# Performance work log

Hardware: AMD Instinct MI355X
Metric: run time of the kernel (lower is better)

Reference implementation:

```python
import jax, jax.numpy as jnp
import numpy as np


def _linear_init(key, fan_in, fan_out):
    bound = 1.0 / np.sqrt(fan_in)
    k1, k2 = jax.random.split(key)
    w = jax.random.uniform(k1, (fan_in, fan_out), jnp.float32, -bound, bound)
    b = jax.random.uniform(k2, (fan_out,), jnp.float32, -bound, bound)
    return w, b


def setup_inputs() -> dict:
    key = jax.random.key(0)
    ks = jax.random.split(key, 8)
    B, T, K, F, H, D = 4, 64, 50, 6, 128, 256
    states = jax.random.normal(ks[0], (B, T, K, F), jnp.float32)
    masks = (jax.random.uniform(ks[1], (B, T, K)) < 0.9).astype(jnp.float32)
    w_a, b_a = _linear_init(ks[2], F, H)              # agent_encoder
    w_r1, b_r1 = _linear_init(ks[3], 2 * H + 3, H)    # relation_encoder layer 1
    w_r2, b_r2 = _linear_init(ks[4], H, H)            # relation_encoder layer 2
    w_g, b_g = _linear_init(ks[5], 2 * H, H)          # graph_aggregation
    w_f1, b_f1 = _linear_init(ks[6], H, D)            # final_encoder layer 1
    w_f2, b_f2 = _linear_init(ks[7], D, D)            # final_encoder layer 2
    return dict(states=states, masks=masks, w_a=w_a, b_a=b_a,
                w_r1=w_r1, b_r1=b_r1, w_r2=w_r2, b_r2=b_r2,
                w_g=w_g, b_g=b_g, w_f1=w_f1, b_f1=b_f1, w_f2=w_f2, b_f2=b_f2)


def _safe_norm(r):
    # sqrt(sum r^2) with well-defined gradient at 0 (torch.norm convention)
    sq = jnp.sum(r * r, axis=-1, keepdims=True)
    return jnp.where(sq == 0, 0.0, jnp.sqrt(jnp.where(sq == 0, 1.0, sq)))


def reference(states, masks, w_a, b_a, w_r1, b_r1, w_r2, b_r2,
              w_g, b_g, w_f1, b_f1, w_f2, b_f2):
    B, T, K, F = states.shape
    H = w_a.shape[1]
    s = states.reshape(B * T, K, F)            # [N,K,F]
    m = masks.reshape(B * T, K)                # [N,K]
    agent_feat = jax.nn.relu(s @ w_a + b_a)    # [N,K,H] (dropout = identity, eval)
    pos = s[..., :2]
    vel = s[..., 2:4]
    # rel[n,i,j] = quantity_j - quantity_i
    rel_pos = pos[:, None, :, :] - pos[:, :, None, :]   # [N,K,K,2]
    rel_vel = vel[:, None, :, :] - vel[:, :, None, :]
    dist = _safe_norm(rel_pos)                          # [N,K,K,1]
    rx, ry = rel_pos[..., 0:1], rel_pos[..., 1:2]
    safe_x = jnp.where((rx == 0) & (ry == 0), 1.0, rx)  # atan2(0,1)=atan2(0,0)=0
    angle = jnp.arctan2(ry, safe_x)
    speed_diff = _safe_norm(rel_vel)
    geo = jnp.concatenate([dist, angle, speed_diff], axis=-1)  # [N,K,K,3]
    # Split the first relation linear instead of materializing the
    # [N,K,K,2H+3] concat: cat([f_i, f_j, geo]) @ w_r1 == f@w_i + f@w_j + geo@w_geo
    x_i = agent_feat @ w_r1[:H]            # [N,K,H]
    x_j = agent_feat @ w_r1[H:2 * H]       # [N,K,H]
    g = geo @ w_r1[2 * H:] + b_r1          # [N,K,K,H]
    h = jax.nn.relu(x_i[:, :, None, :] + x_j[:, None, :, :] + g)
    rel_feat = h @ w_r2 + b_r2             # [N,K,K,H]
    mask_pairs = m[:, :, None] * m[:, None, :]          # [N,i,j]
    rel_feat = rel_feat * mask_pairs[..., None]
    denom = jnp.maximum(mask_pairs.sum(axis=2, keepdims=True), 1.0)  # [N,K,1]
    agg = rel_feat.sum(axis=2) / denom                  # [N,K,H]
    combined = jax.nn.relu(agent_feat @ w_g[:H] + agg @ w_g[H:] + b_g)  # [N,K,H]
    me = m[..., None]
    pooled = (combined * me).sum(axis=1) / jnp.maximum(me.sum(axis=1), 1.0)  # [N,H]
    latent = jax.nn.relu(pooled @ w_f1 + b_f1) @ w_f2 + b_f2                 # [N,D]
    return latent.reshape(B, T, -1)
```

## Files before the change

kernel.cpp:

```cpp
#include <hip/hip_runtime.h>

#define KA 50
#define KP 52
#define H 128
#define D 256
#define NBLK 256
#define BLOCK 1024
#define NG 8
#define RPT 7
#define STRD 136

#define WS_WI 0
#define WS_WJ 32
#define WS_WR2 64
#define WS_WG 96
#define NFRAG 160

typedef __attribute__((ext_vector_type(8))) short bf16x8;
typedef __attribute__((ext_vector_type(4))) float f32x4;

__device__ __forceinline__ float bf2f(unsigned short u) {
  return __uint_as_float(((unsigned)u) << 16);
}
__device__ __forceinline__ unsigned short f2bf(float f) {
  unsigned u = __float_as_uint(f);
  u = (u + 0x7FFFu + ((u >> 16) & 1u)) >> 16;
  return (unsigned short)u;
}
__device__ __forceinline__ float rlf(float v, int l) {
  return __int_as_float(__builtin_amdgcn_readlane(__float_as_int(v), l));
}

__global__ void pack_weights(const float* __restrict__ w_r1,
                             const float* __restrict__ w_r2,
                             const float* __restrict__ w_g,
                             unsigned short* __restrict__ wp) {
  const int t = blockIdx.x * 256 + threadIdx.x;
  if (t >= NFRAG * 64) return;
  const int f = t >> 6, lane = t & 63;
  const float* W; int rowbase, sf;
  if (f < 64)       { W = w_r1; rowbase = (f < 32) ? 0 : 128; sf = f & 31; }
  else if (f < 96)  { W = w_r2; rowbase = 0; sf = f - 64; }
  else              { W = w_g;  rowbase = 0; sf = f - 96; }
  const int kt = sf >> 3, ctl = sf & 7;
  const int col = ctl * 16 + (lane & 15);
  const int k0  = rowbase + kt * 32 + (lane >> 4) * 8;
  unsigned short v[8];
  #pragma unroll
  for (int j = 0; j < 8; ++j) v[j] = f2bf(W[(k0 + j) * H + col]);
  #pragma unroll
  for (int j = 0; j < 8; ++j) wp[(size_t)t * 8 + j] = v[j];
}

struct alignas(16) Smem {
  unsigned short af[KP * STRD];
  unsigned short xi[KP * STRD];
  unsigned short xj[KP * H];
  unsigned short hsum[KP * STRD];
  float red[1024];
  float pooled[H];
  float latent1[D];
  float s[KA][6];
  float m[64];
  float cnta[KP];
  float invden[KP];
  float cnt;
};

__global__ void __launch_bounds__(BLOCK) rpe_kernel(
    const float* __restrict__ states, const float* __restrict__ masks,
    const float* __restrict__ w_a,  const float* __restrict__ b_a,
    const float* __restrict__ w_r1, const float* __restrict__ b_r1,
    const float* __restrict__ b_r2,
    const float* __restrict__ b_g,
    const float* __restrict__ w_f1, const float* __restrict__ b_f1,
    const float* __restrict__ w_f2, const float* __restrict__ b_f2,
    const unsigned short* __restrict__ wp,
    float* __restrict__ out) {
  __shared__ Smem sh;
  const int n = blockIdx.x;
  const int tid = threadIdx.x;
  const int c = tid & (H - 1);
  const int bg = tid >> 7;
  const int wid = tid >> 6, lane = tid & 63;
  const int ct = wid & 7;
  const int rtb = (wid >> 3) * 2;
  const int fr = lane & 15;
  const int fkg = lane >> 4;

  {
    if (tid < KA * 6) ((float*)sh.s)[tid] = states[(size_t)n * (KA * 6) + tid];
    if (tid < 64) sh.m[tid] = (tid < KA) ? masks[(size_t)n * KA + tid] : 0.f;
    if (tid < 2 * H) {
      const int r5 = KA + (tid >> 7), cc = tid & (H - 1);
      sh.af[r5 * STRD + cc] = 0;
      sh.hsum[r5 * STRD + cc] = 0;
    }
  }
  __syncthreads();
  if (tid == 0) {
    float cs = 0.f;
    for (int b = 0; b < KA; ++b) cs += sh.m[b];
    sh.cnt = cs;
  }
  {
    const float bac = b_a[c];
    const float w0 = w_a[0*H+c], w1 = w_a[1*H+c], w2 = w_a[2*H+c];
    const float w3 = w_a[3*H+c], w4 = w_a[4*H+c], w5 = w_a[5*H+c];
    #pragma unroll
    for (int r = 0; r < RPT; ++r) {
      const int a = bg + NG * r;
      if (a < KA) {
        const float* srow = sh.s[a];
        float v = fmaf(srow[0], w0, fmaf(srow[1], w1, fmaf(srow[2], w2,
                  fmaf(srow[3], w3, fmaf(srow[4], w4, fmaf(srow[5], w5, bac))))));
        sh.af[a * STRD + c] = f2bf(fmaxf(v, 0.f));
      }
    }
  }
  __syncthreads();
  if (tid < KP) {
    const float ca = (tid < KA) ? sh.m[tid] * sh.cnt : 0.f;
    sh.cnta[tid] = ca;
    sh.invden[tid] = 1.0f / fmaxf(ca, 1.0f);
  }

  {
    f32x4 ci0 = {0,0,0,0}, ci1 = {0,0,0,0}, cj0 = {0,0,0,0}, cj1 = {0,0,0,0};
    #pragma unroll
    for (int kt = 0; kt < 4; ++kt) {
      const bf16x8 Bi = *(const bf16x8*)&wp[(size_t)((WS_WI + kt*8 + ct) * 64 + lane) * 8];
      const bf16x8 Bj = *(const bf16x8*)&wp[(size_t)((WS_WJ + kt*8 + ct) * 64 + lane) * 8];
      const bf16x8 A0 = *(const bf16x8*)&sh.af[(rtb*16 + fr) * STRD + kt*32 + fkg*8];
      const bf16x8 A1 = *(const bf16x8*)&sh.af[((rtb+1)*16 + fr) * STRD + kt*32 + fkg*8];
      ci0 = __builtin_amdgcn_mfma_f32_16x16x32_bf16(A0, Bi, ci0, 0, 0, 0);
      ci1 = __builtin_amdgcn_mfma_f32_16x16x32_bf16(A1, Bi, ci1, 0, 0, 0);
      cj0 = __builtin_amdgcn_mfma_f32_16x16x32_bf16(A0, Bj, cj0, 0, 0, 0);
      cj1 = __builtin_amdgcn_mfma_f32_16x16x32_bf16(A1, Bj, cj1, 0, 0, 0);
    }
    const int col = ct * 16 + fr;
    #pragma unroll
    for (int rt2 = 0; rt2 < 2; ++rt2) {
      const f32x4 vi = rt2 ? ci1 : ci0;
      const f32x4 vj = rt2 ? cj1 : cj0;
      #pragma unroll
      for (int g = 0; g < 4; ++g) {
        const int r = (rtb + rt2) * 16 + fkg * 4 + g;
        if (r < KP) {
          sh.xi[r * STRD + col] = f2bf(vi[g]);
          sh.xj[r * H + col]    = f2bf(vj[g]);
        }
      }
    }
  }
  __syncthreads();

  {
    const int c0 = 2 * lane;
    const float wgd0  = w_r1[256*H + c0], wgd1  = w_r1[256*H + c0+1];
    const float wgan0 = w_r1[257*H + c0], wgan1 = w_r1[257*H + c0+1];
    const float wgs0  = w_r1[258*H + c0], wgs1  = w_r1[258*H + c0+1];
    const float br10  = b_r1[c0],         br11  = b_r1[c0+1];
    const int bl = (lane < KA) ? lane : (KA - 1);
    const float pbx = sh.s[bl][0], pby = sh.s[bl][1];
    const float pvx = sh.s[bl][2], pvy = sh.s[bl][3];
    const float mb  = sh.m[lane];

    float dG[3], aG[3], sG[3], b0v[3], b1v[3], h0v[3], h1v[3];
    #pragma unroll
    for (int r = 0; r < 3; ++r) {
      const int ar = wid + 16 * r;
      const float rx  = pbx - sh.s[ar][0], ry  = pby - sh.s[ar][1];
      const float dvx = pvx - sh.s[ar][2], dvy = pvy - sh.s[ar][3];
      dG[r] = sqrtf(fmaf(rx, rx, ry * ry));
      const float sx = (rx == 0.f && ry == 0.f) ? 1.f : rx;
      aG[r] = atan2f(ry, sx);
      sG[r] = sqrtf(fmaf(dvx, dvx, dvy * dvy));
      const unsigned xip = *(const unsigned*)&sh.xi[ar * STRD + c0];
      b0v[r] = bf2f((unsigned short)xip) + br10;
      b1v[r] = bf2f((unsigned short)(xip >> 16)) + br11;
      h0v[r] = 0.f; h1v[r] = 0.f;
    }
    #pragma unroll 10
    for (int b = 0; b < KA; ++b) {
      const unsigned xjp = *(const unsigned*)&sh.xj[b * H + c0];
      const float xj0 = __uint_as_float(xjp << 16);
      const float xj1 = __uint_as_float(xjp & 0xFFFF0000u);
      const float mm = rlf(mb, b);
      #pragma unroll
      for (int r = 0; r < 3; ++r) {
        const float dd = rlf(dG[r], b), aa = rlf(aG[r], b), ss = rlf(sG[r], b);
        float t0 = fmaf(dd, wgd0, b0v[r]); t0 = fmaf(aa, wgan0, t0);
        t0 = fmaf(ss, wgs0, t0);  t0 += xj0;
        float t1 = fmaf(dd, wgd1, b1v[r]); t1 = fmaf(aa, wgan1, t1);
        t1 = fmaf(ss, wgs1, t1);  t1 += xj1;
        h0v[r] = fmaf(mm, fmaxf(t0, 0.f), h0v[r]);
        h1v[r] = fmaf(mm, fmaxf(t1, 0.f), h1v[r]);
      }
    }
    #pragma unroll
    for (int r = 0; r < 3; ++r) {
      const int ar = wid + 16 * r;
      const float ma = sh.m[ar];
      const float g0 = h0v[r] * ma, g1 = h1v[r] * ma;
      *(unsigned*)&sh.hsum[ar * STRD + c0] =
          (unsigned)f2bf(g0) | ((unsigned)f2bf(g1) << 16);
    }
    if (wid < 2) {
      const int ar = 48 + wid;
      const float rx  = pbx - sh.s[ar][0], ry  = pby - sh.s[ar][1];
      const float dvx = pvx - sh.s[ar][2], dvy = pvy - sh.s[ar][3];
      const float dGt = sqrtf(fmaf(rx, rx, ry * ry));
      const float sx  = (rx == 0.f && ry == 0.f) ? 1.f : rx;
      const float aGt = atan2f(ry, sx);
      const float sGt = sqrtf(fmaf(dvx, dvx, dvy * dvy));
      const unsigned xip = *(const unsigned*)&sh.xi[ar * STRD + c0];
      const float b0t = bf2f((unsigned short)xip) + br10;
      const float b1t = bf2f((unsigned short)(xip >> 16)) + br11;
      float h0 = 0.f, h1 = 0.f;
      #pragma unroll 10
      for (int b = 0; b < KA; ++b) {
        const unsigned xjp = *(const unsigned*)&sh.xj[b * H + c0];
        const float xj0 = __uint_as_float(xjp << 16);
        const float xj1 = __uint_as_float(xjp & 0xFFFF0000u);
        const float mm = rlf(mb, b);
        const float dd = rlf(dGt, b), aa = rlf(aGt, b), ss = rlf(sGt, b);
        float t0 = fmaf(dd, wgd0, b0t); t0 = fmaf(aa, wgan0, t0);
        t0 = fmaf(ss, wgs0, t0);  t0 += xj0;
        float t1 = fmaf(dd, wgd1, b1t); t1 = fmaf(aa, wgan1, t1);
        t1 = fmaf(ss, wgs1, t1);  t1 += xj1;
        h0 = fmaf(mm, fmaxf(t0, 0.f), h0);
        h1 = fmaf(mm, fmaxf(t1, 0.f), h1);
      }
      const float ma = sh.m[ar];
      const float g0 = h0 * ma, g1 = h1 * ma;
      *(unsigned*)&sh.hsum[ar * STRD + c0] =
          (unsigned)f2bf(g0) | ((unsigned)f2bf(g1) << 16);
    }
  }
  __syncthreads();

  {
    f32x4 a0 = {0,0,0,0}, a1 = {0,0,0,0};
    #pragma unroll
    for (int kt = 0; kt < 4; ++kt) {
      const bf16x8 B = *(const bf16x8*)&wp[(size_t)((WS_WR2 + kt*8 + ct) * 64 + lane) * 8];
      const bf16x8 A0 = *(const bf16x8*)&sh.hsum[(rtb*16 + fr) * STRD + kt*32 + fkg*8];
      const bf16x8 A1 = *(const bf16x8*)&sh.hsum[((rtb+1)*16 + fr) * STRD + kt*32 + fkg*8];
      a0 = __builtin_amdgcn_mfma_f32_16x16x32_bf16(A0, B, a0, 0, 0, 0);
      a1 = __builtin_amdgcn_mfma_f32_16x16x32_bf16(A1, B, a1, 0, 0, 0);
    }
    const int col = ct * 16 + fr;
    const float br2c = b_r2[col];
    #pragma unroll
    for (int rt2 = 0; rt2 < 2; ++rt2) {
      const f32x4 v = rt2 ? a1 : a0;
      #pragma unroll
      for (int g = 0; g < 4; ++g) {
        const int r = (rtb + rt2) * 16 + fkg * 4 + g;
        if (r < KP) {
          const float val = fmaf(sh.cnta[r], br2c, v[g]) * sh.invden[r];
          sh.xi[r * STRD + col] = f2bf(val);
        }
      }
    }
  }
  __syncthreads();

  {
    f32x4 a0 = {0,0,0,0}, a1 = {0,0,0,0};
    #pragma unroll
    for (int kt = 0; kt < 4; ++kt) {
      const bf16x8 B = *(const bf16x8*)&wp[(size_t)((WS_WG + kt*8 + ct) * 64 + lane) * 8];
      const bf16x8 A0 = *(const bf16x8*)&sh.af[(rtb*16 + fr) * STRD + kt*32 + fkg*8];
      const bf16x8 A1 = *(const bf16x8*)&sh.af[((rtb+1)*16 + fr) * STRD + kt*32 + fkg*8];
      a0 = __builtin_amdgcn_mfma_f32_16x16x32_bf16(A0, B, a0, 0, 0, 0);
      a1 = __builtin_amdgcn_mfma_f32_16x16x32_bf16(A1, B, a1, 0, 0, 0);
    }
    #pragma unroll
    for (int kt = 0; kt < 4; ++kt) {
      const bf16x8 B = *(const bf16x8*)&wp[(size_t)((WS_WG + (kt+4)*8 + ct) * 64 + lane) * 8];
      const bf16x8 A0 = *(const bf16x8*)&sh.xi[(rtb*16 + fr) * STRD + kt*32 + fkg*8];
      const bf16x8 A1 = *(const bf16x8*)&sh.xi[((rtb+1)*16 + fr) * STRD + kt*32 + fkg*8];
      a0 = __builtin_amdgcn_mfma_f32_16x16x32_bf16(A0, B, a0, 0, 0, 0);
      a1 = __builtin_amdgcn_mfma_f32_16x16x32_bf16(A1, B, a1, 0, 0, 0);
    }
    const int col = ct * 16 + fr;
    const float bgc = b_g[col];
    float pv = 0.f;
    #pragma unroll
    for (int rt2 = 0; rt2 < 2; ++rt2) {
      const f32x4 v = rt2 ? a1 : a0;
      #pragma unroll
      for (int g = 0; g < 4; ++g) {
        const int r = (rtb + rt2) * 16 + fkg * 4 + g;
        if (r < KA) {
          pv = fmaf(sh.m[r], fmaxf(v[g] + bgc, 0.f), pv);
        }
      }
    }
    pv += __shfl_xor(pv, 16);
    pv += __shfl_xor(pv, 32);
    if (lane < 16) sh.red[(wid >> 3) * H + col] = pv;
  }
  __syncthreads();
  if (tid < H) {
    const float invp = 1.0f / fmaxf(sh.cnt, 1.0f);
    sh.pooled[tid] = (sh.red[tid] + sh.red[H + tid]) * invp;
  }
  __syncthreads();

  {
    const int d  = tid & (D - 1);
    const int hh = tid >> 8;
    const float* wf = w_f1 + d;
    float acc = 0.f;
    const int k0 = hh * 32;
    #pragma unroll 8
    for (int k = 0; k < 32; ++k)
      acc = fmaf(sh.pooled[k0 + k], wf[(k0 + k) * D], acc);
    sh.red[hh * D + d] = acc;
  }
  __syncthreads();
  if (tid < D) {
    sh.latent1[tid] = fmaxf(sh.red[tid] + sh.red[D + tid] +
                            sh.red[2*D + tid] + sh.red[3*D + tid] +
                            b_f1[tid], 0.f);
  }
  __syncthreads();

  {
    const int d  = tid & (D - 1);
    const int hh = tid >> 8;
    const float* wf = w_f2 + d;
    float acc = 0.f;
    const int k0 = hh * 64;
    #pragma unroll 8
    for (int k = 0; k < 64; ++k)
      acc = fmaf(sh.latent1[k0 + k], wf[(k0 + k) * D], acc);
    sh.red[hh * D + d] = acc;
  }
  __syncthreads();
  if (tid < D) {
    out[(size_t)n * D + tid] = sh.red[tid] + sh.red[D + tid] +
                               sh.red[2*D + tid] + sh.red[3*D + tid] +
                               b_f2[tid];
  }
}

extern "C" void kernel_launch(void* const* d_in, const int* in_sizes, int n_in,
                              void* d_out, int out_size, void* d_ws, size_t ws_size,
                              hipStream_t stream) {
  const float* states = (const float*)d_in[0];
  const float* masks  = (const float*)d_in[1];
  const float* w_a  = (const float*)d_in[2];
  const float* b_a  = (const float*)d_in[3];
  const float* w_r1 = (const float*)d_in[4];
  const float* b_r1 = (const float*)d_in[5];
  const float* w_r2 = (const float*)d_in[6];
  const float* b_r2 = (const float*)d_in[7];
  const float* w_g  = (const float*)d_in[8];
  const float* b_g  = (const float*)d_in[9];
  const float* w_f1 = (const float*)d_in[10];
  const float* b_f1 = (const float*)d_in[11];
  const float* w_f2 = (const float*)d_in[12];
  const float* b_f2 = (const float*)d_in[13];
  float* out = (float*)d_out;
  unsigned short* wp = (unsigned short*)d_ws;

  hipLaunchKernelGGL(pack_weights, dim3((NFRAG * 64 + 255) / 256), dim3(256), 0, stream,
                     w_r1, w_r2, w_g, wp);
  hipLaunchKernelGGL(rpe_kernel, dim3(NBLK), dim3(BLOCK), 0, stream,
                     states, masks, w_a, b_a, w_r1, b_r1, b_r2,
                     b_g, w_f1, b_f1, w_f2, b_f2, wp, out);
}
```

Measured before the change: 42.47 us.

## Hoist weight loads and geometry math ahead of barriers to overlap latency

Global weight loads (w_a, relation geometry weights, MFMA B fragments, final-encoder weights) are issued earlier, before the barriers that precede their use. Pairwise geometry (distance, atan2, speed) is computed during the agent-encoder phase instead of after the x_i/x_j MFMA phase. The first half of the graph-aggregation MFMA is merged into the w_r2 MFMA loop, and the mask count uses a wave shuffle reduction instead of a serial loop on one thread. The aim is to hide global-memory latency and shorten the serial sync stages, at the cost of many more live registers (96 floats for w_f1/w_f2 plus B fragments) in a 1024-thread block, which risks spills.

```diff
diff --git a/kernel.cpp b/kernel.cpp
--- a/kernel.cpp
+++ b/kernel.cpp
@@ -87,6 +87,16 @@
   const int rtb = (wid >> 3) * 2;
   const int fr = lane & 15;
   const int fkg = lane >> 4;
+  const int col = ct * 16 + fr;
+
+  const float bac = b_a[c];
+  const float wa0 = w_a[0*H+c], wa1 = w_a[1*H+c], wa2 = w_a[2*H+c];
+  const float wa3 = w_a[3*H+c], wa4 = w_a[4*H+c], wa5 = w_a[5*H+c];
+  const int c0 = 2 * lane;
+  const float wgd0  = w_r1[256*H + c0], wgd1  = w_r1[256*H + c0+1];
+  const float wgan0 = w_r1[257*H + c0], wgan1 = w_r1[257*H + c0+1];
+  const float wgs0  = w_r1[258*H + c0], wgs1  = w_r1[258*H + c0+1];
+  const float br10  = b_r1[c0],         br11  = b_r1[c0+1];
 
   {
     if (tid < KA * 6) ((float*)sh.s)[tid] = states[(size_t)n * (KA * 6) + tid];
@@ -98,25 +108,56 @@
     }
   }
   __syncthreads();
-  if (tid == 0) {
-    float cs = 0.f;
-    for (int b = 0; b < KA; ++b) cs += sh.m[b];
-    sh.cnt = cs;
-  }
-  {
-    const float bac = b_a[c];
-    const float w0 = w_a[0*H+c], w1 = w_a[1*H+c], w2 = w_a[2*H+c];
-    const float w3 = w_a[3*H+c], w4 = w_a[4*H+c], w5 = w_a[5*H+c];
+  if (wid == 0) {
+    float v = sh.m[lane];
+    v += __shfl_xor(v, 1);  v += __shfl_xor(v, 2);  v += __shfl_xor(v, 4);
+    v += __shfl_xor(v, 8);  v += __shfl_xor(v, 16); v += __shfl_xor(v, 32);
+    if (lane == 0) sh.cnt = v;
+  }
+
+  const int bl = (lane < KA) ? lane : (KA - 1);
+  const float pbx = sh.s[bl][0], pby = sh.s[bl][1];
+  const float pvx = sh.s[bl][2], pvy = sh.s[bl][3];
+  const float mb  = sh.m[lane];
+  float dG[3], aG[3], sG[3];
+  #pragma unroll
+  for (int r = 0; r < 3; ++r) {
+    const int ar = wid + 16 * r;
+    const float rx  = pbx - sh.s[ar][0], ry  = pby - sh.s[ar][1];
+    const float dvx = pvx - sh.s[ar][2], dvy = pvy - sh.s[ar][3];
+    dG[r] = sqrtf(fmaf(rx, rx, ry * ry));
+    const float sx = (rx == 0.f && ry == 0.f) ? 1.f : rx;
+    aG[r] = atan2f(ry, sx);
+    sG[r] = sqrtf(fmaf(dvx, dvx, dvy * dvy));
+  }
+  float dGt = 0.f, aGt = 0.f, sGt = 0.f;
+  if (wid < 2) {
+    const int ar = 48 + wid;
+    const float rx  = pbx - sh.s[ar][0], ry  = pby - sh.s[ar][1];
+    const float dvx = pvx - sh.s[ar][2], dvy = pvy - sh.s[ar][3];
+    dGt = sqrtf(fmaf(rx, rx, ry * ry));
+    const float sx = (rx == 0.f && ry == 0.f) ? 1.f : rx;
+    aGt = atan2f(ry, sx);
+    sGt = sqrtf(fmaf(dvx, dvx, dvy * dvy));
+  }
+
+  {
     #pragma unroll
     for (int r = 0; r < RPT; ++r) {
       const int a = bg + NG * r;
       if (a < KA) {
         const float* srow = sh.s[a];
-        float v = fmaf(srow[0], w0, fmaf(srow[1], w1, fmaf(srow[2], w2,
-                  fmaf(srow[3], w3, fmaf(srow[4], w4, fmaf(srow[5], w5, bac))))));
+        float v = fmaf(srow[0], wa0, fmaf(srow[1], wa1, fmaf(srow[2], wa2,
+                  fmaf(srow[3], wa3, fmaf(srow[4], wa4, fmaf(srow[5], wa5, bac))))));
         sh.af[a * STRD + c] = f2bf(fmaxf(v, 0.f));
       }
     }
+  }
+  bf16x8 Bi[4], Bj[4];
+  #pragma unroll
+  for (int kt = 0; kt < 4; ++kt) {
+    Bi[kt] = *(const bf16x8*)&wp[(size_t)((WS_WI + kt*8 + ct) * 64 + lane) * 8];
+    Bj[kt] = *(const bf16x8*)&wp[(size_t)((WS_WJ + kt*8 + ct) * 64 + lane) * 8];
   }
   __syncthreads();
   if (tid < KP) {
@@ -129,16 +170,13 @@
     f32x4 ci0 = {0,0,0,0}, ci1 = {0,0,0,0}, cj0 = {0,0,0,0}, cj1 = {0,0,0,0};
     #pragma unroll
     for (int kt = 0; kt < 4; ++kt) {
-      const bf16x8 Bi = *(const bf16x8*)&wp[(size_t)((WS_WI + kt*8 + ct) * 64 + lane) * 8];
-      const bf16x8 Bj = *(const bf16x8*)&wp[(size_t)((WS_WJ + kt*8 + ct) * 64 + lane) * 8];
       const bf16x8 A0 = *(const bf16x8*)&sh.af[(rtb*16 + fr) * STRD + kt*32 + fkg*8];
       const bf16x8 A1 = *(const bf16x8*)&sh.af[((rtb+1)*16 + fr) * STRD + kt*32 + fkg*8];
-      ci0 = __builtin_amdgcn_mfma_f32_16x16x32_bf16(A0, Bi, ci0, 0, 0, 0);
-      ci1 = __builtin_amdgcn_mfma_f32_16x16x32_bf16(A1, Bi, ci1, 0, 0, 0);
-      cj0 = __builtin_amdgcn_mfma_f32_16x16x32_bf16(A0, Bj, cj0, 0, 0, 0);
-      cj1 = __builtin_amdgcn_mfma_f32_16x16x32_bf16(A1, Bj, cj1, 0, 0, 0);
-    }
-    const int col = ct * 16 + fr;
+      ci0 = __builtin_amdgcn_mfma_f32_16x16x32_bf16(A0, Bi[kt], ci0, 0, 0, 0);
+      ci1 = __builtin_amdgcn_mfma_f32_16x16x32_bf16(A1, Bi[kt], ci1, 0, 0, 0);
+      cj0 = __builtin_amdgcn_mfma_f32_16x16x32_bf16(A0, Bj[kt], cj0, 0, 0, 0);
+      cj1 = __builtin_amdgcn_mfma_f32_16x16x32_bf16(A1, Bj[kt], cj1, 0, 0, 0);
+    }
     #pragma unroll
     for (int rt2 = 0; rt2 < 2; ++rt2) {
       const f32x4 vi = rt2 ? ci1 : ci0;
@@ -156,26 +194,10 @@
   __syncthreads();
 
   {
-    const int c0 = 2 * lane;
-    const float wgd0  = w_r1[256*H + c0], wgd1  = w_r1[256*H + c0+1];
-    const float wgan0 = w_r1[257*H + c0], wgan1 = w_r1[257*H + c0+1];
-    const float wgs0  = w_r1[258*H + c0], wgs1  = w_r1[258*H + c0+1];
-    const float br10  = b_r1[c0],         br11  = b_r1[c0+1];
-    const int bl = (lane < KA) ? lane : (KA - 1);
-    const float pbx = sh.s[bl][0], pby = sh.s[bl][1];
-    const float pvx = sh.s[bl][2], pvy = sh.s[bl][3];
-    const float mb  = sh.m[lane];
-
-    float dG[3], aG[3], sG[3], b0v[3], b1v[3], h0v[3], h1v[3];
+    float b0v[3], b1v[3], h0v[3], h1v[3];
     #pragma unroll
     for (int r = 0; r < 3; ++r) {
       const int ar = wid + 16 * r;
-      const float rx  = pbx - sh.s[ar][0], ry  = pby - sh.s[ar][1];
-      const float dvx = pvx - sh.s[ar][2], dvy = pvy - sh.s[ar][3];
-      dG[r] = sqrtf(fmaf(rx, rx, ry * ry));
-      const float sx = (rx == 0.f && ry == 0.f) ? 1.f : rx;
-      aG[r] = atan2f(ry, sx);
-      sG[r] = sqrtf(fmaf(dvx, dvx, dvy * dvy));
       const unsigned xip = *(const unsigned*)&sh.xi[ar * STRD + c0];
       b0v[r] = bf2f((unsigned short)xip) + br10;
       b1v[r] = bf2f((unsigned short)(xip >> 16)) + br11;
@@ -208,12 +230,6 @@
     }
     if (wid < 2) {
       const int ar = 48 + wid;
-      const float rx  = pbx - sh.s[ar][0], ry  = pby - sh.s[ar][1];
-      const float dvx = pvx - sh.s[ar][2], dvy = pvy - sh.s[ar][3];
-      const float dGt = sqrtf(fmaf(rx, rx, ry * ry));
-      const float sx  = (rx == 0.f && ry == 0.f) ? 1.f : rx;
-      const float aGt = atan2f(ry, sx);
-      const float sGt = sqrtf(fmaf(dvx, dvx, dvy * dvy));
       const unsigned xip = *(const unsigned*)&sh.xi[ar * STRD + c0];
       const float b0t = bf2f((unsigned short)xip) + br10;
       const float b1t = bf2f((unsigned short)(xip >> 16)) + br11;
@@ -240,17 +256,22 @@
   }
   __syncthreads();
 
+  f32x4 p0 = {0,0,0,0}, p1 = {0,0,0,0};
   {
     f32x4 a0 = {0,0,0,0}, a1 = {0,0,0,0};
     #pragma unroll
     for (int kt = 0; kt < 4; ++kt) {
-      const bf16x8 B = *(const bf16x8*)&wp[(size_t)((WS_WR2 + kt*8 + ct) * 64 + lane) * 8];
-      const bf16x8 A0 = *(const bf16x8*)&sh.hsum[(rtb*16 + fr) * STRD + kt*32 + fkg*8];
-      const bf16x8 A1 = *(const bf16x8*)&sh.hsum[((rtb+1)*16 + fr) * STRD + kt*32 + fkg*8];
-      a0 = __builtin_amdgcn_mfma_f32_16x16x32_bf16(A0, B, a0, 0, 0, 0);
-      a1 = __builtin_amdgcn_mfma_f32_16x16x32_bf16(A1, B, a1, 0, 0, 0);
-    }
-    const int col = ct * 16 + fr;
+      const bf16x8 B4 = *(const bf16x8*)&wp[(size_t)((WS_WR2 + kt*8 + ct) * 64 + lane) * 8];
+      const bf16x8 A0h = *(const bf16x8*)&sh.hsum[(rtb*16 + fr) * STRD + kt*32 + fkg*8];
+      const bf16x8 A1h = *(const bf16x8*)&sh.hsum[((rtb+1)*16 + fr) * STRD + kt*32 + fkg*8];
+      a0 = __builtin_amdgcn_mfma_f32_16x16x32_bf16(A0h, B4, a0, 0, 0, 0);
+      a1 = __builtin_amdgcn_mfma_f32_16x16x32_bf16(A1h, B4, a1, 0, 0, 0);
+      const bf16x8 B5 = *(const bf16x8*)&wp[(size_t)((WS_WG + kt*8 + ct) * 64 + lane) * 8];
+      const bf16x8 A0a = *(const bf16x8*)&sh.af[(rtb*16 + fr) * STRD + kt*32 + fkg*8];
+      const bf16x8 A1a = *(const bf16x8*)&sh.af[((rtb+1)*16 + fr) * STRD + kt*32 + fkg*8];
+      p0 = __builtin_amdgcn_mfma_f32_16x16x32_bf16(A0a, B5, p0, 0, 0, 0);
+      p1 = __builtin_amdgcn_mfma_f32_16x16x32_bf16(A1a, B5, p1, 0, 0, 0);
+    }
     const float br2c = b_r2[col];
     #pragma unroll
     for (int rt2 = 0; rt2 < 2; ++rt2) {
@@ -268,29 +289,19 @@
   __syncthreads();
 
   {
-    f32x4 a0 = {0,0,0,0}, a1 = {0,0,0,0};
-    #pragma unroll
-    for (int kt = 0; kt < 4; ++kt) {
-      const bf16x8 B = *(const bf16x8*)&wp[(size_t)((WS_WG + kt*8 + ct) * 64 + lane) * 8];
-      const bf16x8 A0 = *(const bf16x8*)&sh.af[(rtb*16 + fr) * STRD + kt*32 + fkg*8];
-      const bf16x8 A1 = *(const bf16x8*)&sh.af[((rtb+1)*16 + fr) * STRD + kt*32 + fkg*8];
-      a0 = __builtin_amdgcn_mfma_f32_16x16x32_bf16(A0, B, a0, 0, 0, 0);
-      a1 = __builtin_amdgcn_mfma_f32_16x16x32_bf16(A1, B, a1, 0, 0, 0);
-    }
     #pragma unroll
     for (int kt = 0; kt < 4; ++kt) {
       const bf16x8 B = *(const bf16x8*)&wp[(size_t)((WS_WG + (kt+4)*8 + ct) * 64 + lane) * 8];
       const bf16x8 A0 = *(const bf16x8*)&sh.xi[(rtb*16 + fr) * STRD + kt*32 + fkg*8];
       const bf16x8 A1 = *(const bf16x8*)&sh.xi[((rtb+1)*16 + fr) * STRD + kt*32 + fkg*8];
-      a0 = __builtin_amdgcn_mfma_f32_16x16x32_bf16(A0, B, a0, 0, 0, 0);
-      a1 = __builtin_amdgcn_mfma_f32_16x16x32_bf16(A1, B, a1, 0, 0, 0);
-    }
-    const int col = ct * 16 + fr;
+      p0 = __builtin_amdgcn_mfma_f32_16x16x32_bf16(A0, B, p0, 0, 0, 0);
+      p1 = __builtin_amdgcn_mfma_f32_16x16x32_bf16(A1, B, p1, 0, 0, 0);
+    }
     const float bgc = b_g[col];
     float pv = 0.f;
     #pragma unroll
     for (int rt2 = 0; rt2 < 2; ++rt2) {
-      const f32x4 v = rt2 ? a1 : a0;
+      const f32x4 v = rt2 ? p1 : p0;
       #pragma unroll
       for (int g = 0; g < 4; ++g) {
         const int r = (rtb + rt2) * 16 + fkg * 4 + g;
@@ -303,6 +314,15 @@
     pv += __shfl_xor(pv, 32);
     if (lane < 16) sh.red[(wid >> 3) * H + col] = pv;
   }
+  const int d67 = tid & (D - 1);
+  const int hh67 = tid >> 8;
+  float wf1r[32];
+  {
+    const float* wf = w_f1 + d67;
+    const int k06 = hh67 * 32;
+    #pragma unroll
+    for (int k = 0; k < 32; ++k) wf1r[k] = wf[(k06 + k) * D];
+  }
   __syncthreads();
   if (tid < H) {
     const float invp = 1.0f / fmaxf(sh.cnt, 1.0f);
@@ -311,15 +331,19 @@
   __syncthreads();
 
   {
-    const int d  = tid & (D - 1);
-    const int hh = tid >> 8;
-    const float* wf = w_f1 + d;
     float acc = 0.f;
-    const int k0 = hh * 32;
-    #pragma unroll 8
+    const int k06 = hh67 * 32;
+    #pragma unroll
     for (int k = 0; k < 32; ++k)
-      acc = fmaf(sh.pooled[k0 + k], wf[(k0 + k) * D], acc);
-    sh.red[hh * D + d] = acc;
+      acc = fmaf(sh.pooled[k06 + k], wf1r[k], acc);
+    sh.red[hh67 * D + d67] = acc;
+  }
+  float wf2r[64];
+  {
+    const float* wf = w_f2 + d67;
+    const int k07 = hh67 * 64;
+    #pragma unroll
+    for (int k = 0; k < 64; ++k) wf2r[k] = wf[(k07 + k) * D];
   }
   __syncthreads();
   if (tid < D) {
@@ -330,15 +354,12 @@
   __syncthreads();
 
   {
-    const int d  = tid & (D - 1);
-    const int hh = tid >> 8;
-    const float* wf = w_f2 + d;
     float acc = 0.f;
-    const int k0 = hh * 64;
-    #pragma unroll 8
+    const int k07 = hh67 * 64;
+    #pragma unroll
     for (int k = 0; k < 64; ++k)
-      acc = fmaf(sh.latent1[k0 + k], wf[(k0 + k) * D], acc);
-    sh.red[hh * D + d] = acc;
+      acc = fmaf(sh.latent1[k07 + k], wf2r[k], acc);
+    sh.red[hh67 * D + d67] = acc;
   }
   __syncthreads();
   if (tid < D) {
```

After: 42.59 us. No clear change (+0.3%).
